# Optimization experiments

Hardware: AMD Instinct MI355X
Metric: run time of the kernel (lower is better)

## Reference

```python
import jax, jax.numpy as jnp
import numpy as np

HIDDEN_DIM = 512
RADIUS = 128


def rel_pos_indexes(seq_len_q: int, seq_len_k: int, radius: int):
    # (i - j) clamped to [-radius, radius], shifted to [0, 2*radius]
    i = jnp.arange(seq_len_k)[None, :]   # [1, Sk]
    j = jnp.arange(seq_len_q)[:, None]   # [Sq, 1]
    return jnp.clip(i - j, -radius, radius) + radius  # [Sq, Sk] int


def setup_inputs() -> dict:
    key = jax.random.key(0)
    kq, kk, kv, ke = jax.random.split(key, 4)
    B, Sq, Sk, d = 4, 2048, 2048, HIDDEN_DIM
    Q = jax.random.normal(kq, (B, Sq, d), dtype=jnp.float32)
    K = jax.random.normal(kk, (B, Sk, d), dtype=jnp.float32)
    V = jax.random.normal(kv, (B, Sk, d), dtype=jnp.float32)
    # learned relative-position embedding table: (2R+1, d)
    rel_embeds = jax.random.normal(ke, (2 * RADIUS + 1, d), dtype=jnp.float32)
    return {"Q": Q, "K": K, "V": V, "rel_embeds": rel_embeds}


def reference(Q, K, V, rel_embeds):
    B, Sq, d = Q.shape
    Sk = K.shape[1]
    normalizer = jnp.asarray(d ** 0.5, dtype=Q.dtype)
    # content scores: [B, Sq, Sk]
    energy = jnp.einsum('bqd,bkd->bqk', Q, K)
    # relative scores: Q against the (2R+1) relative embeddings -> [B, Sq, 2R+1]
    Q_rel = jnp.einsum('bqd,rd->bqr', Q, rel_embeds)
    idx = rel_pos_indexes(Sq, Sk, RADIUS)  # [Sq, Sk]
    # gather along last dim per query row (same index map for every batch)
    rel_shift = jnp.take_along_axis(Q_rel, idx[None, :, :].repeat(B, axis=0), axis=2)
    energy = (energy + rel_shift) / normalizer
    attn = jax.nn.softmax(energy, axis=2)
    Z = jnp.einsum('bqk,bkd->bqd', attn, V)
    return attn, Z
```

## Files before the change

kernel.cpp:

```cpp
#include <hip/hip_runtime.h>

#define BATCH 4
#define SQL 2048
#define SKL 2048
#define DIM 512
#define NR 257
#define NRP 288
#define RAD 128

typedef __bf16 bf16x8 __attribute__((ext_vector_type(8)));
typedef float f32x4 __attribute__((ext_vector_type(4)));
typedef unsigned short u16;
typedef u16 u16x4 __attribute__((ext_vector_type(4)));
typedef u16 u16x8 __attribute__((ext_vector_type(8)));

__device__ inline u16 f2bf(float x) {
  union { float f; unsigned u; } v; v.f = x;
  unsigned r = v.u + 0x7FFF + ((v.u >> 16) & 1);
  return (u16)(r >> 16);
}

__device__ inline void glds16(const u16* g, const u16* l) {
  __builtin_amdgcn_global_load_lds(
      (const __attribute__((address_space(1))) void*)g,
      (__attribute__((address_space(3))) void*)l, 16, 0, 0);
}

__global__ __launch_bounds__(256) void prep_mem_kernel(const float* __restrict__ Q,
                                                       const float* __restrict__ K,
                                                       const float* __restrict__ V,
                                                       const float* __restrict__ rel,
                                                       u16x4* __restrict__ Qb,
                                                       u16x4* __restrict__ Kb,
                                                       u16* __restrict__ relb,
                                                       u16* __restrict__ Vt) {
  __shared__ float tile[32][33];
  int bid = blockIdx.x, tid = threadIdx.x;
  if (bid < 8192) {
    const f32x4* src = (bid < 4096) ? (const f32x4*)Q : (const f32x4*)K;
    u16x4* dst = (bid < 4096) ? Qb : Kb;
    int i = (bid & 4095) * 256 + tid;
    f32x4 f = src[i];
    u16x4 o;
#pragma unroll
    for (int e = 0; e < 4; e++) o[e] = f2bf(f[e]);
    dst[i] = o;
  } else if (bid < 8768) {
    int i = (bid - 8192) * 256 + tid;
    int r = i >> 9;
    relb[i] = (r < NR) ? f2bf(rel[i]) : (u16)0;
  } else {
    int t = bid - 8768;
    int b = t >> 10, rem = t & 1023;
    int k0 = (rem & 63) * 32, d0 = (rem >> 6) * 32;
    int tx = tid & 31, ty = tid >> 5;
#pragma unroll
    for (int r = 0; r < 4; r++)
      tile[ty + r * 8][tx] = V[((long)b * SKL + k0 + ty + r * 8) * DIM + d0 + tx];
    __syncthreads();
#pragma unroll
    for (int r = 0; r < 4; r++)
      Vt[((long)b * DIM + d0 + ty + r * 8) * SKL + k0 + tx] = f2bf(tile[tx][ty + r * 8]);
  }
}

__global__ __launch_bounds__(256) void qrel_kernel(const u16* __restrict__ Qb,
                                                   const u16* __restrict__ relb,
                                                   float* __restrict__ Qrel) {
  int tid = threadIdx.x;
  int wave = tid >> 6, lane = tid & 63;
  int m0 = blockIdx.x * 64 + wave * 16;
  int j0 = blockIdx.y * 2;
  int fr = lane & 15, fk = (lane >> 4) * 8;
  f32x4 acc[2] = {};
  const u16* qrow = Qb + (long)(m0 + fr) * DIM + fk;
  const u16* r0 = relb + (long)(j0 * 16 + fr) * DIM + fk;
  const u16* r1 = r0 + 16 * DIM;
  for (int k0 = 0; k0 < DIM; k0 += 32) {
    bf16x8 a = *(const bf16x8*)(qrow + k0);
    bf16x8 b0 = *(const bf16x8*)(r0 + k0);
    bf16x8 b1 = *(const bf16x8*)(r1 + k0);
    acc[0] = __builtin_amdgcn_mfma_f32_16x16x32_bf16(a, b0, acc[0], 0, 0, 0);
    acc[1] = __builtin_amdgcn_mfma_f32_16x16x32_bf16(a, b1, acc[1], 0, 0, 0);
  }
  int cr = (lane >> 4) * 4, cc = lane & 15;
#pragma unroll
  for (int t = 0; t < 2; t++)
#pragma unroll
    for (int r = 0; r < 4; r++)
      Qrel[(long)(m0 + cr + r) * NRP + (j0 + t) * 16 + cc] = acc[t][r];
}

__global__ __launch_bounds__(256) void energy_kernel(const u16* __restrict__ Qb,
                                                     const u16* __restrict__ Kb,
                                                     u16* __restrict__ S) {
  int b = blockIdx.z;
  int m0 = blockIdx.y * 128;
  int n0 = blockIdx.x * 128;
  const u16* A = Qb + (long)b * SQL * DIM;
  const u16* Bp = Kb + (long)b * SKL * DIM;
  __shared__ u16 lds[32768];
  u16* As0 = lds;          u16* Bs0 = lds + 8192;
  u16* As1 = lds + 16384;  u16* Bs1 = lds + 24576;
  int tid = threadIdx.x;
  int wave = tid >> 6, lane = tid & 63;
  int wm = (wave >> 1) * 64, wn = (wave & 1) * 64;
  int fr = lane & 15, g = lane >> 4;
  int srow = lane >> 3;
  int scol = ((lane & 7) ^ srow) * 8;
  f32x4 acc[4][4] = {};

  auto stage = [&](u16* dA, u16* dB, int k0) {
#pragma unroll
    for (int c = 0; c < 4; c++) {
      int r = wave * 32 + c * 8;
      glds16(A + (long)(m0 + r + srow) * DIM + k0 + scol, dA + r * 64);
      glds16(Bp + (long)(n0 + r + srow) * DIM + k0 + scol, dB + r * 64);
    }
  };
  auto compute = [&](const u16* Asb, const u16* Bsb) {
#pragma unroll
    for (int s = 0; s < 2; s++) {
      bf16x8 af[4], bfv[4];
#pragma unroll
      for (int i = 0; i < 4; i++) {
        int row = wm + i * 16 + fr;
        int cb = (s * 64 + g * 16) ^ ((row & 7) << 4);
        af[i] = *(const bf16x8*)(Asb + row * 64 + (cb >> 1));
      }
#pragma unroll
      for (int j = 0; j < 4; j++) {
        int row = wn + j * 16 + fr;
        int cb = (s * 64 + g * 16) ^ ((row & 7) << 4);
        bfv[j] = *(const bf16x8*)(Bsb + row * 64 + (cb >> 1));
      }
#pragma unroll
      for (int i = 0; i < 4; i++)
#pragma unroll
        for (int j = 0; j < 4; j++)
          acc[i][j] = __builtin_amdgcn_mfma_f32_16x16x32_bf16(af[i], bfv[j], acc[i][j], 0, 0, 0);
    }
  };

  const int NT = DIM / 64;
  stage(As0, Bs0, 0);
  __syncthreads();
  for (int t = 0; t < NT; t += 2) {
    if (t + 1 < NT) stage(As1, Bs1, (t + 1) * 64);
    compute(As0, Bs0);
    __syncthreads();
    if (t + 1 < NT) {
      if (t + 2 < NT) stage(As0, Bs0, (t + 2) * 64);
      compute(As1, Bs1);
      __syncthreads();
    }
  }

  const float inv_norm = 0.04419417382415922f;
  int cr = (lane >> 4) * 4, cc = lane & 15;
#pragma unroll
  for (int i = 0; i < 4; i++) {
#pragma unroll
    for (int r = 0; r < 4; r++) {
      int q = m0 + wm + i * 16 + cr + r;
      u16* sr = S + ((long)b * SQL + q) * SKL;
#pragma unroll
      for (int j = 0; j < 4; j++)
        sr[n0 + wn + j * 16 + cc] = f2bf(acc[i][j][r] * inv_norm);
    }
  }
}

__global__ __launch_bounds__(256) void softmax_kernel(u16* __restrict__ S,
                                                      const float* __restrict__ Qrel,
                                                      float* __restrict__ attn) {
  long row = blockIdx.x;
  int q = (int)(row & (SQL - 1));
  u16* srow = S + row * SKL;
  float* arow = attn + row * SKL;
  int tid = threadIdx.x;
  int wave = tid >> 6, lane = tid & 63;
  __shared__ float qlds[NR];
  __shared__ float red[4];
  const float inv_norm = 0.04419417382415922f;
  const float* qr = Qrel + row * NRP;
  qlds[tid] = qr[tid] * inv_norm;
  if (tid == 0) qlds[256] = qr[256] * inv_norm;
  bf16x8 v = *(const bf16x8*)(srow + tid * 8);
  __syncthreads();
  float f[8];
  int kb = tid * 8 - q + RAD;
#pragma unroll
  for (int e = 0; e < 8; e++) {
    int idx = kb + e;
    idx = idx < 0 ? 0 : (idx > 2 * RAD ? 2 * RAD : idx);
    f[e] = (float)v[e] + qlds[idx];
  }
  float m = -1e30f;
#pragma unroll
  for (int e = 0; e < 8; e++) m = fmaxf(m, f[e]);
  for (int o = 32; o > 0; o >>= 1) m = fmaxf(m, __shfl_xor(m, o));
  if (lane == 0) red[wave] = m;
  __syncthreads();
  m = fmaxf(fmaxf(red[0], red[1]), fmaxf(red[2], red[3]));
  __syncthreads();
  float s = 0.0f;
  float e8[8];
#pragma unroll
  for (int e = 0; e < 8; e++) { e8[e] = __expf(f[e] - m); s += e8[e]; }
  for (int o = 32; o > 0; o >>= 1) s += __shfl_xor(s, o);
  if (lane == 0) red[wave] = s;
  __syncthreads();
  s = red[0] + red[1] + red[2] + red[3];
  float inv = 1.0f / s;
  f32x4 o0, o1;
  u16x8 pb;
#pragma unroll
  for (int e = 0; e < 4; e++) {
    float p = e8[e] * inv;
    o0[e] = p; pb[e] = f2bf(p);
  }
#pragma unroll
  for (int e = 0; e < 4; e++) {
    float p = e8[e + 4] * inv;
    o1[e] = p; pb[e + 4] = f2bf(p);
  }
  *(f32x4*)(arow + tid * 8) = o0;
  *(f32x4*)(arow + tid * 8 + 4) = o1;
  *(u16x8*)(srow + tid * 8) = pb;
}

__global__ __launch_bounds__(256) void z_kernel(const u16* __restrict__ S,
                                                const u16* __restrict__ Vt,
                                                float* __restrict__ Z) {
  int b = blockIdx.z;
  int m0 = blockIdx.y * 64;
  int n0 = blockIdx.x * 128;
  const u16* A = S + (long)b * SQL * SKL;
  const u16* Bp = Vt + (long)b * DIM * SKL;
  __shared__ u16 lds[24576];
  u16* As0 = lds;          u16* Bs0 = lds + 4096;
  u16* As1 = lds + 12288;  u16* Bs1 = lds + 16384;
  int tid = threadIdx.x;
  int wave = tid >> 6, lane = tid & 63;
  int wm = (wave >> 1) * 32, wn = (wave & 1) * 64;
  int fr = lane & 15, g = lane >> 4;
  int srow = lane >> 3;
  int scol = ((lane & 7) ^ srow) * 8;
  f32x4 acc[2][4] = {};

  auto stage = [&](u16* dA, u16* dB, int k0) {
#pragma unroll
    for (int c = 0; c < 2; c++) {
      int r = wave * 16 + c * 8;
      glds16(A + (long)(m0 + r + srow) * SKL + k0 + scol, dA + r * 64);
    }
#pragma unroll
    for (int c = 0; c < 4; c++) {
      int r = wave * 32 + c * 8;
      glds16(Bp + (long)(n0 + r + srow) * SKL + k0 + scol, dB + r * 64);
    }
  };
  auto compute = [&](const u16* Asb, const u16* Bsb) {
#pragma unroll
    for (int s = 0; s < 2; s++) {
      bf16x8 af[2], bfv[4];
#pragma unroll
      for (int i = 0; i < 2; i++) {
        int row = wm + i * 16 + fr;
        int cb = (s * 64 + g * 16) ^ ((row & 7) << 4);
        af[i] = *(const bf16x8*)(Asb + row * 64 + (cb >> 1));
      }
#pragma unroll
      for (int j = 0; j < 4; j++) {
        int row = wn + j * 16 + fr;
        int cb = (s * 64 + g * 16) ^ ((row & 7) << 4);
        bfv[j] = *(const bf16x8*)(Bsb + row * 64 + (cb >> 1));
      }
#pragma unroll
      for (int i = 0; i < 2; i++)
#pragma unroll
        for (int j = 0; j < 4; j++)
          acc[i][j] = __builtin_amdgcn_mfma_f32_16x16x32_bf16(af[i], bfv[j], acc[i][j], 0, 0, 0);
    }
  };

  const int NT = SKL / 64;
  stage(As0, Bs0, 0);
  __syncthreads();
  for (int t = 0; t < NT; t += 2) {
    if (t + 1 < NT) stage(As1, Bs1, (t + 1) * 64);
    compute(As0, Bs0);
    __syncthreads();
    if (t + 1 < NT) {
      if (t + 2 < NT) stage(As0, Bs0, (t + 2) * 64);
      compute(As1, Bs1);
      __syncthreads();
    }
  }

  int cr = (lane >> 4) * 4, cc = lane & 15;
#pragma unroll
  for (int i = 0; i < 2; i++)
#pragma unroll
    for (int r = 0; r < 4; r++) {
      int q = m0 + wm + i * 16 + cr + r;
      float* zrow = Z + ((long)b * SQL + q) * DIM;
#pragma unroll
      for (int j = 0; j < 4; j++)
        zrow[n0 + wn + j * 16 + cc] = acc[i][j][r];
    }
}


extern "C" void kernel_launch(void* const* d_in, const int* in_sizes, int n_in,
                              void* d_out, int out_size, void* d_ws, size_t ws_size,
                              hipStream_t stream) {
  const float* Q = (const float*)d_in[0];
  const float* K = (const float*)d_in[1];
  const float* V = (const float*)d_in[2];
  const float* rel = (const float*)d_in[3];
  float* attn = (float*)d_out;
  float* Z = attn + (long)BATCH * SQL * SKL;

  char* ws = (char*)d_ws;
  u16* Qb   = (u16*)ws;
  u16* Kb   = (u16*)(ws + 8388608);
  u16* Vt   = (u16*)(ws + 16777216);
  u16* relb = (u16*)(ws + 25165824);
  float* Qrel = (float*)(ws + 25460736);
  u16* S    = (u16*)(ws + 34897920);

  prep_mem_kernel<<<12864, 256, 0, stream>>>(Q, K, V, rel, (u16x4*)Qb, (u16x4*)Kb, relb, Vt);
  qrel_kernel<<<dim3(128, 9), 256, 0, stream>>>(Qb, relb, Qrel);
  energy_kernel<<<dim3(16, 16, BATCH), 256, 0, stream>>>(Qb, Kb, S);
  softmax_kernel<<<8192, 256, 0, stream>>>(S, Qrel, attn);
  z_kernel<<<dim3(4, 32, BATCH), 256, 0, stream>>>(S, Vt, Z);
}
```

Measured before the change: 232.7 us.

## Enlarge energy GEMM tiles to 256x256 with 8 waves and finer-grained pipelining

```diff
diff --git a/kernel.cpp b/kernel.cpp
--- a/kernel.cpp
+++ b/kernel.cpp
@@ -91,84 +91,109 @@
       Qrel[(long)(m0 + cr + r) * NRP + (j0 + t) * 16 + cc] = acc[t][r];
 }
 
-__global__ __launch_bounds__(256) void energy_kernel(const u16* __restrict__ Qb,
-                                                     const u16* __restrict__ Kb,
-                                                     u16* __restrict__ S) {
+__global__ __launch_bounds__(512, 2) void energy_kernel(const u16* __restrict__ Qb,
+                                                        const u16* __restrict__ Kb,
+                                                        u16* __restrict__ S) {
+  __shared__ u16 lds[65536];
   int b = blockIdx.z;
-  int m0 = blockIdx.y * 128;
-  int n0 = blockIdx.x * 128;
+  int m0 = blockIdx.y * 256, n0 = blockIdx.x * 256;
   const u16* A = Qb + (long)b * SQL * DIM;
   const u16* Bp = Kb + (long)b * SKL * DIM;
-  __shared__ u16 lds[32768];
-  u16* As0 = lds;          u16* Bs0 = lds + 8192;
-  u16* As1 = lds + 16384;  u16* Bs1 = lds + 24576;
   int tid = threadIdx.x;
   int wave = tid >> 6, lane = tid & 63;
-  int wm = (wave >> 1) * 64, wn = (wave & 1) * 64;
+  int wr = wave >> 2, wc = wave & 3;
   int fr = lane & 15, g = lane >> 4;
-  int srow = lane >> 3;
-  int scol = ((lane & 7) ^ srow) * 8;
-  f32x4 acc[4][4] = {};
-
-  auto stage = [&](u16* dA, u16* dB, int k0) {
-#pragma unroll
-    for (int c = 0; c < 4; c++) {
-      int r = wave * 32 + c * 8;
-      glds16(A + (long)(m0 + r + srow) * DIM + k0 + scol, dA + r * 64);
-      glds16(Bp + (long)(n0 + r + srow) * DIM + k0 + scol, dB + r * 64);
-    }
-  };
-  auto compute = [&](const u16* Asb, const u16* Bsb) {
-#pragma unroll
-    for (int s = 0; s < 2; s++) {
-      bf16x8 af[4], bfv[4];
-#pragma unroll
-      for (int i = 0; i < 4; i++) {
-        int row = wm + i * 16 + fr;
-        int cb = (s * 64 + g * 16) ^ ((row & 7) << 4);
-        af[i] = *(const bf16x8*)(Asb + row * 64 + (cb >> 1));
-      }
-#pragma unroll
-      for (int j = 0; j < 4; j++) {
-        int row = wn + j * 16 + fr;
-        int cb = (s * 64 + g * 16) ^ ((row & 7) << 4);
-        bfv[j] = *(const bf16x8*)(Bsb + row * 64 + (cb >> 1));
-      }
-#pragma unroll
-      for (int i = 0; i < 4; i++)
-#pragma unroll
-        for (int j = 0; j < 4; j++)
-          acc[i][j] = __builtin_amdgcn_mfma_f32_16x16x32_bf16(af[i], bfv[j], acc[i][j], 0, 0, 0);
-    }
-  };
+  int srow8 = lane >> 3;
+  int scol = ((lane & 7) ^ srow8) * 8;
+
+  f32x4 acc[4][2][4] = {};
+  bf16x8 bB[4][2];
+
+#define STA(slot, tt, q) do { \
+    int rb_ = (q) * 32 + (wave & 3) * 8 + (wave >> 2) * 128; \
+    glds16(A + (long)(m0 + rb_ + srow8) * DIM + (tt) * 64 + scol, \
+           lds + (slot) * 32768 + rb_ * 64); \
+  } while (0)
+#define STB(slot, tt, p) do { \
+    int rb_ = (p) * 64 + wave * 8; \
+    glds16(Bp + (long)(n0 + rb_ + srow8) * DIM + (tt) * 64 + scol, \
+           lds + (slot) * 32768 + 16384 + rb_ * 64); \
+  } while (0)
+#define LOADB(slot) do { \
+    const u16* base_ = lds + (slot) * 32768 + 16384; \
+    _Pragma("unroll") for (int jb = 0; jb < 4; jb++) { \
+      _Pragma("unroll") for (int ks = 0; ks < 2; ks++) { \
+        int row_ = wc * 64 + jb * 16 + fr; \
+        int cb_ = (ks * 64 + g * 16) ^ ((row_ & 7) << 4); \
+        bB[jb][ks] = *(const bf16x8*)(base_ + row_ * 64 + (cb_ >> 1)); \
+      } \
+    } \
+  } while (0)
+#define QUAD(slot, q) do { \
+    const u16* baseA_ = lds + (slot) * 32768; \
+    bf16x8 a_[2][2]; \
+    _Pragma("unroll") for (int rb = 0; rb < 2; rb++) { \
+      _Pragma("unroll") for (int ks = 0; ks < 2; ks++) { \
+        int row_ = wr * 128 + (q) * 32 + rb * 16 + fr; \
+        int cb_ = (ks * 64 + g * 16) ^ ((row_ & 7) << 4); \
+        a_[rb][ks] = *(const bf16x8*)(baseA_ + row_ * 64 + (cb_ >> 1)); \
+      } \
+    } \
+    __builtin_amdgcn_s_setprio(1); \
+    _Pragma("unroll") for (int rb = 0; rb < 2; rb++) \
+    _Pragma("unroll") for (int jb = 0; jb < 4; jb++) \
+    _Pragma("unroll") for (int ks = 0; ks < 2; ks++) \
+      acc[q][rb][jb] = __builtin_amdgcn_mfma_f32_16x16x32_bf16(a_[rb][ks], bB[jb][ks], acc[q][rb][jb], 0, 0, 0); \
+    __builtin_amdgcn_s_setprio(0); \
+  } while (0)
 
   const int NT = DIM / 64;
-  stage(As0, Bs0, 0);
-  __syncthreads();
-  for (int t = 0; t < NT; t += 2) {
-    if (t + 1 < NT) stage(As1, Bs1, (t + 1) * 64);
-    compute(As0, Bs0);
-    __syncthreads();
+  STA(0, 0, 0); STA(0, 0, 1); STA(0, 0, 2); STA(0, 0, 3);
+  STB(0, 0, 0); STB(0, 0, 1); STB(0, 0, 2); STB(0, 0, 3);
+  STA(1, 1, 0); STA(1, 1, 1); STA(1, 1, 2);
+  asm volatile("s_waitcnt vmcnt(3)" ::: "memory");
+  asm volatile("s_barrier" ::: "memory");
+
+  for (int t = 0; t < NT; ++t) {
+    int cs = t & 1, ns = cs ^ 1;
     if (t + 1 < NT) {
-      if (t + 2 < NT) stage(As0, Bs0, (t + 2) * 64);
-      compute(As1, Bs1);
-      __syncthreads();
-    }
-  }
+      STA(ns, t + 1, 3);
+      STB(ns, t + 1, 0); STB(ns, t + 1, 1); STB(ns, t + 1, 2); STB(ns, t + 1, 3);
+    }
+    LOADB(cs);
+    QUAD(cs, 0);
+    asm volatile("s_barrier" ::: "memory");
+    if (t + 2 < NT) STA(cs, t + 2, 0);
+    QUAD(cs, 1);
+    asm volatile("s_barrier" ::: "memory");
+    if (t + 2 < NT) STA(cs, t + 2, 1);
+    QUAD(cs, 2);
+    asm volatile("s_barrier" ::: "memory");
+    if (t + 2 < NT) STA(cs, t + 2, 2);
+    QUAD(cs, 3);
+    if (t + 2 < NT) asm volatile("s_waitcnt vmcnt(3)" ::: "memory");
+    else            asm volatile("s_waitcnt vmcnt(0)" ::: "memory");
+    asm volatile("s_barrier" ::: "memory");
+  }
+#undef STA
+#undef STB
+#undef LOADB
+#undef QUAD
 
   const float inv_norm = 0.04419417382415922f;
   int cr = (lane >> 4) * 4, cc = lane & 15;
 #pragma unroll
-  for (int i = 0; i < 4; i++) {
-#pragma unroll
-    for (int r = 0; r < 4; r++) {
-      int q = m0 + wm + i * 16 + cr + r;
-      u16* sr = S + ((long)b * SQL + q) * SKL;
-#pragma unroll
-      for (int j = 0; j < 4; j++)
-        sr[n0 + wn + j * 16 + cc] = f2bf(acc[i][j][r] * inv_norm);
-    }
-  }
+  for (int q = 0; q < 4; q++)
+#pragma unroll
+    for (int rb = 0; rb < 2; rb++)
+#pragma unroll
+      for (int r = 0; r < 4; r++) {
+        int row = m0 + wr * 128 + q * 32 + rb * 16 + cr + r;
+        u16* sr = S + ((long)b * SQL + row) * SKL;
+#pragma unroll
+        for (int jb = 0; jb < 4; jb++)
+          sr[n0 + wc * 64 + jb * 16 + cc] = f2bf(acc[q][rb][jb][r] * inv_norm);
+      }
 }
 
 __global__ __launch_bounds__(256) void softmax_kernel(u16* __restrict__ S,
@@ -333,7 +358,7 @@
 
   prep_mem_kernel<<<12864, 256, 0, stream>>>(Q, K, V, rel, (u16x4*)Qb, (u16x4*)Kb, relb, Vt);
   qrel_kernel<<<dim3(128, 9), 256, 0, stream>>>(Qb, relb, Qrel);
-  energy_kernel<<<dim3(16, 16, BATCH), 256, 0, stream>>>(Qb, Kb, S);
+  energy_kernel<<<dim3(8, 8, BATCH), 512, 0, stream>>>(Qb, Kb, S);
   softmax_kernel<<<8192, 256, 0, stream>>>(S, Qrel, attn);
   z_kernel<<<dim3(4, 32, BATCH), 256, 0, stream>>>(S, Vt, Z);
 }
```

After: 225.1 us. 3.3% less time.
